# Kernel tuning notes

Hardware: AMD Instinct MI355X
Metric: run time of the kernel (lower is better)

Reference implementation:

```python
import jax, jax.numpy as jnp
import numpy as np

N_NODES = 50000
N_EDGES = 1600000
IN_DIM = 128
HID = 128
SHARED = 64
N_GRAPHS = 2048


def setup_inputs() -> dict:
    key = jax.random.key(0)
    ks = jax.random.split(key, 16)
    x = jax.random.normal(ks[0], (N_NODES, IN_DIM), dtype=jnp.float32)
    edge_index = jax.random.randint(ks[1], (2, N_EDGES), 0, N_NODES, dtype=jnp.int64)
    batch = jnp.sort(jax.random.randint(ks[2], (N_NODES,), 0, N_GRAPHS, dtype=jnp.int64))

    def lin(k, fan_in, fan_out):
        bound = 1.0 / np.sqrt(fan_in)
        kw, kb = jax.random.split(k)
        W = jax.random.uniform(kw, (fan_in, fan_out), minval=-bound, maxval=bound, dtype=jnp.float32)
        b = jax.random.uniform(kb, (fan_out,), minval=-bound, maxval=bound, dtype=jnp.float32)
        return W, b

    W1a, b1a = lin(ks[3], IN_DIM, HID)
    W1b, b1b = lin(ks[4], HID, HID)
    W2a, b2a = lin(ks[5], HID, HID)
    W2b, b2b = lin(ks[6], HID, HID)
    Ws, bs = lin(ks[7], HID, SHARED)
    WlS, blS = lin(ks[8], SHARED, 1)
    WlP, blP = lin(ks[9], SHARED, 1)
    WnR, bnR = lin(ks[10], SHARED, 1)
    return dict(x=x, edge_index=edge_index, batch=batch,
                W1a=W1a, b1a=b1a, W1b=W1b, b1b=b1b,
                W2a=W2a, b2a=b2a, W2b=W2b, b2b=b2b,
                Ws=Ws, bs=bs, WlS=WlS, blS=blS, WlP=WlP, blP=blP, WnR=WnR, bnR=bnR)


def gin_conv(x, src, dst, Wa, ba, Wb, bb):
    # GINConv (eps=0): h_i = MLP(x_i + sum_{j->i} x_j)
    agg = jax.ops.segment_sum(x[src], dst, num_segments=N_NODES)
    h = x + agg
    h = jax.nn.relu(h @ Wa + ba)
    return h @ Wb + bb


def reference(x, edge_index, batch, W1a, b1a, W1b, b1b, W2a, b2a, W2b, b2b,
              Ws, bs, WlS, blS, WlP, blP, WnR, bnR):
    src, dst = edge_index[0], edge_index[1]
    h = jax.nn.relu(gin_conv(x, src, dst, W1a, b1a, W1b, b1b))
    h = jax.nn.relu(gin_conv(h, src, dst, W2a, b2a, W2b, b2b))
    # global mean pool over graph ids
    sums = jax.ops.segment_sum(h, batch, num_segments=N_GRAPHS)
    counts = jax.ops.segment_sum(jnp.ones((h.shape[0],), h.dtype), batch, num_segments=N_GRAPHS)
    pooled = sums / jnp.maximum(counts, 1.0)[:, None]
    g = jax.nn.relu(pooled @ Ws + bs)
    out_logS = (g @ WlS + blS)[:, 0]
    out_logP = (g @ WlP + blP)[:, 0]
    out_NR = (g @ WnR + bnR)[:, 0]
    return (out_logS, out_logP, out_NR)
```

## Files before the change

### kernel.cpp

```cpp
#include <hip/hip_runtime.h>
#include <hip/hip_bf16.h>


#define IN_DIM 128
#define NFINE 128
#define BIN_EPB 4096
#define SRCCH 16
#define NSLOT 6400
#define SPT 13

typedef float  f32x4  __attribute__((ext_vector_type(4)));
typedef short  bf16x4 __attribute__((ext_vector_type(4)));
typedef short  bf16x8 __attribute__((ext_vector_type(8)));

__device__ __forceinline__ unsigned short bf16_rne(float v) {
    unsigned u = __float_as_uint(v);
    unsigned t = u + 0x7fffu + ((u >> 16) & 1u);
    return (unsigned short)(t >> 16);
}


__global__ __launch_bounds__(256) void f32_to_bf16_kernel(
    const float4* __restrict__ in, uint4* __restrict__ out, int n8)
{
    int i = blockIdx.x * 256 + threadIdx.x;
    if (i >= n8) return;
    float4 a = in[i * 2];
    float4 b = in[i * 2 + 1];
    float v[8] = {a.x, a.y, a.z, a.w, b.x, b.y, b.z, b.w};
    unsigned r[4];
#pragma unroll
    for (int j = 0; j < 4; ++j)
        r[j] = (unsigned)bf16_rne(v[j * 2]) | ((unsigned)bf16_rne(v[j * 2 + 1]) << 16);
    out[i] = make_uint4(r[0], r[1], r[2], r[3]);
}


__global__ __launch_bounds__(256) void conv_weights_kernel(
    const float* __restrict__ W0, const float* __restrict__ W1,
    const float* __restrict__ W2, const float* __restrict__ W3,
    unsigned short* __restrict__ Wh, unsigned short* __restrict__ Wl)
{
    int m   = blockIdx.x >> 6;
    int idx = (blockIdx.x & 63) * 256 + threadIdx.x;
    const float* W = (m == 0) ? W0 : (m == 1) ? W1 : (m == 2) ? W2 : W3;
    int k = idx >> 7, n = idx & 127;
    float v = W[idx];
    unsigned short hh = bf16_rne(v);
    float hf = __uint_as_float(((unsigned)hh) << 16);
    unsigned short ll = bf16_rne(v - hf);
    Wh[m * 16384 + n * 128 + k] = hh;
    Wl[m * 16384 + n * 128 + k] = ll;
}


__global__ __launch_bounds__(256) void bin_kernel(
    const int* __restrict__ src, const int* __restrict__ dst,
    int2* __restrict__ buckets, int* __restrict__ bcur,
    int n_edges, int n_nodes, int cap)
{
    __shared__ int cnt[NFINE];
    __shared__ int base[NFINE];
    for (int i = threadIdx.x; i < NFINE; i += 256) cnt[i] = 0;
    __syncthreads();

    const int e0 = blockIdx.x * BIN_EPB + threadIdx.x * 16;
    int ne = n_edges - e0;
    if (ne < 0) ne = 0;
    if (ne > 16) ne = 16;

    int d[16], s[16], off[16];
    if (ne == 16) {
#pragma unroll
        for (int q = 0; q < 4; ++q) {
            int4 dv = *(const int4*)(dst + e0 + q * 4);
            int4 sv = *(const int4*)(src + e0 + q * 4);
            d[q * 4 + 0] = dv.x; d[q * 4 + 1] = dv.y;
            d[q * 4 + 2] = dv.z; d[q * 4 + 3] = dv.w;
            s[q * 4 + 0] = sv.x; s[q * 4 + 1] = sv.y;
            s[q * 4 + 2] = sv.z; s[q * 4 + 3] = sv.w;
        }
    } else {
#pragma unroll
        for (int j = 0; j < 16; ++j) {
            d[j] = (j < ne) ? dst[e0 + j] : 0;
            s[j] = (j < ne) ? src[e0 + j] : 0;
        }
    }
#pragma unroll
    for (int j = 0; j < 16; ++j)
        if (j < ne) {
            int b = (int)(((long long)d[j] * NFINE) / n_nodes);
            off[j] = atomicAdd(&cnt[b], 1);
        }
    __syncthreads();
    for (int i = threadIdx.x; i < NFINE; i += 256)
        base[i] = atomicAdd(&bcur[i], cnt[i]);
    __syncthreads();
#pragma unroll
    for (int j = 0; j < 16; ++j)
        if (j < ne) {
            int b = (int)(((long long)d[j] * NFINE) / n_nodes);
            buckets[(size_t)b * cap + base[b] + off[j]] = make_int2(d[j], s[j]);
        }
}

__global__ __launch_bounds__(512) void csr_fused_kernel(
    const int2* __restrict__ buckets, const int* __restrict__ bcnt,
    int* __restrict__ row_start, int* __restrict__ csr_src,
    int cap, int n_nodes, int n_edges)
{
    __shared__ int bc[NFINE];
    __shared__ int h[NSLOT];
    __shared__ int tsum[512];
    __shared__ int bbase_s;

    const int b = blockIdx.x;
    const int t = threadIdx.x;
    const int lo_n = (int)(((long long)b * n_nodes + NFINE - 1) / NFINE);
    const int hi_n = (int)(((long long)(b + 1) * n_nodes + NFINE - 1) / NFINE);
    const int sl = hi_n - lo_n;

    if (t < NFINE) bc[t] = bcnt[t];
    for (int i = t; i < NSLOT; i += 512) h[i] = 0;
    __syncthreads();
    if (t == 0) {
        int s = 0;
        for (int i = 0; i < b; ++i) s += bc[i];
        bbase_s = s;
    }
    const int nb = bc[b];
    const int2* bp = buckets + (size_t)b * cap;
    __syncthreads();

    for (int i = t; i < nb; i += 512) {
        int2 e = bp[i];
        int key = (e.x - lo_n) * SRCCH + (int)(((long long)e.y * SRCCH) / n_nodes);
        atomicAdd(&h[key], 1);
    }
    __syncthreads();

    int base = 0;
#pragma unroll
    for (int j = 0; j < SPT; ++j) {
        int slot = t * SPT + j;
        if (slot < NSLOT) {
            int v = h[slot];
            h[slot] = base;
            base += v;
        }
    }
    tsum[t] = base;
    __syncthreads();
    for (int off = 1; off < 512; off <<= 1) {
        int tmp = (t >= off) ? tsum[t - off] : 0;
        __syncthreads();
        tsum[t] += tmp;
        __syncthreads();
    }
    int texcl = tsum[t] - base + bbase_s;
#pragma unroll
    for (int j = 0; j < SPT; ++j) {
        int slot = t * SPT + j;
        if (slot < NSLOT) h[slot] += texcl;
    }
    __syncthreads();
    for (int i = t; i < sl; i += 512) row_start[lo_n + i] = h[i * SRCCH];
    if (b == NFINE - 1 && t == 0) row_start[n_nodes] = n_edges;
    __syncthreads();

    for (int i = t; i < nb; i += 512) {
        int2 e = bp[i];
        int key = (e.x - lo_n) * SRCCH + (int)(((long long)e.y * SRCCH) / n_nodes);
        csr_src[atomicAdd(&h[key], 1)] = e.y;
    }
}


__device__ __forceinline__ void add_row8(float acc[8], uint4 r) {
    union { unsigned u; float f; } c;
    c.u = r.x << 16;         acc[0] += c.f;
    c.u = r.x & 0xffff0000u; acc[1] += c.f;
    c.u = r.y << 16;         acc[2] += c.f;
    c.u = r.y & 0xffff0000u; acc[3] += c.f;
    c.u = r.z << 16;         acc[4] += c.f;
    c.u = r.z & 0xffff0000u; acc[5] += c.f;
    c.u = r.w << 16;         acc[6] += c.f;
    c.u = r.w & 0xffff0000u; acc[7] += c.f;
}

__global__ __launch_bounds__(256) void gather_agg_bf16_kernel(
    const float* __restrict__ xf,
    const uint4* __restrict__ xb,
    const int* __restrict__ row_start, const int* __restrict__ csr_src,
    float* __restrict__ out, int n_nodes)
{
    int blk = blockIdx.x;
    int nfull = (gridDim.x >> 5) << 5;
    int group;
    if (blk < nfull) {
        int x = blk & 7;
        int q = blk >> 3;
        group = ((q >> 2) << 5) + (x << 2) + (q & 3);
    } else {
        group = blk;
    }

    int node = group * 16 + (threadIdx.x >> 4);
    int lane = threadIdx.x & 15;
    if (node >= n_nodes) return;
    int lo = row_start[node];
    int hi = row_start[node + 1];

    const f32x4* xfr = (const f32x4*)(xf + (size_t)node * IN_DIM + lane * 8);
    f32x4 a0 = xfr[0];
    f32x4 a1 = xfr[1];
    float acc[8] = {a0.x, a0.y, a0.z, a0.w, a1.x, a1.y, a1.z, a1.w};

    int e = lo;
    for (; e + 3 < hi; e += 4) {
        int s0 = csr_src[e];
        int s1 = csr_src[e + 1];
        int s2 = csr_src[e + 2];
        int s3 = csr_src[e + 3];
        uint4 r0 = xb[(size_t)s0 * 16 + lane];
        uint4 r1 = xb[(size_t)s1 * 16 + lane];
        uint4 r2 = xb[(size_t)s2 * 16 + lane];
        uint4 r3 = xb[(size_t)s3 * 16 + lane];
        add_row8(acc, r0);
        add_row8(acc, r1);
        add_row8(acc, r2);
        add_row8(acc, r3);
    }
    for (; e < hi; ++e) {
        uint4 r = xb[(size_t)csr_src[e] * 16 + lane];
        add_row8(acc, r);
    }

    f32x4* op = (f32x4*)(out + (size_t)node * IN_DIM + lane * 8);
    op[0] = (f32x4){acc[0], acc[1], acc[2], acc[3]};
    op[1] = (f32x4){acc[4], acc[5], acc[6], acc[7]};
}

#define HSTRIDE 132

template <bool EMIT_BF16>
__global__ __launch_bounds__(256) void fused_mlp_kernel(
    const float* __restrict__ A,
    const unsigned short* __restrict__ Wa_h, const unsigned short* __restrict__ Wa_l,
    const float* __restrict__ ba,
    const unsigned short* __restrict__ Wb_h, const unsigned short* __restrict__ Wb_l,
    const float* __restrict__ bb,
    float* __restrict__ C, unsigned short* __restrict__ Cb, int M)
{
    __shared__ __align__(16) unsigned short Hh[64][HSTRIDE];
    __shared__ __align__(16) unsigned short Hl[64][HSTRIDE];

    const int t    = threadIdx.x;
    const int wave = t >> 6;
    const int lane = t & 63;
    const int l15  = lane & 15;
    const int quad = lane >> 4;
    const int rw   = (wave & 1) * 32;
    const int cw   = (wave >> 1) * 64;
    const int row0 = blockIdx.x * 64 + rw;

    f32x4 acc[2][4];
#pragma unroll
    for (int ti = 0; ti < 2; ++ti)
#pragma unroll
        for (int ct = 0; ct < 4; ++ct) acc[ti][ct] = {0.f, 0.f, 0.f, 0.f};

    {
        int ar0 = row0 + l15;
        int ar1 = row0 + 16 + l15;
        const float* ap0 = A + (size_t)((ar0 < M) ? ar0 : (M - 1)) * IN_DIM + quad * 8;
        const float* ap1 = A + (size_t)((ar1 < M) ? ar1 : (M - 1)) * IN_DIM + quad * 8;
#pragma unroll
        for (int k0 = 0; k0 < IN_DIM; k0 += 32) {
            bf16x8 ah[2], al[2];
#pragma unroll
            for (int ti = 0; ti < 2; ++ti) {
                const float* ap = ti ? ap1 : ap0;
                f32x4 v0 = *(const f32x4*)(ap + k0);
                f32x4 v1 = *(const f32x4*)(ap + k0 + 4);
                float v[8] = {v0.x, v0.y, v0.z, v0.w, v1.x, v1.y, v1.z, v1.w};
                unsigned short h[8], l[8];
#pragma unroll
                for (int j = 0; j < 8; ++j) {
                    unsigned short hh = bf16_rne(v[j]);
                    h[j] = hh;
                    l[j] = bf16_rne(v[j] - __uint_as_float(((unsigned)hh) << 16));
                }
                ah[ti] = *(const bf16x8*)h;
                al[ti] = *(const bf16x8*)l;
            }
#pragma unroll
            for (int ct = 0; ct < 4; ++ct) {
                const size_t woff = (size_t)(cw + ct * 16 + l15) * IN_DIM + k0 + quad * 8;
                bf16x8 wh = *(const bf16x8*)(Wa_h + woff);
                bf16x8 wl = *(const bf16x8*)(Wa_l + woff);
                acc[0][ct] = __builtin_amdgcn_mfma_f32_16x16x32_bf16(ah[0], wh, acc[0][ct], 0, 0, 0);
                acc[1][ct] = __builtin_amdgcn_mfma_f32_16x16x32_bf16(ah[1], wh, acc[1][ct], 0, 0, 0);
                acc[0][ct] = __builtin_amdgcn_mfma_f32_16x16x32_bf16(al[0], wh, acc[0][ct], 0, 0, 0);
                acc[1][ct] = __builtin_amdgcn_mfma_f32_16x16x32_bf16(al[1], wh, acc[1][ct], 0, 0, 0);
                acc[0][ct] = __builtin_amdgcn_mfma_f32_16x16x32_bf16(ah[0], wl, acc[0][ct], 0, 0, 0);
                acc[1][ct] = __builtin_amdgcn_mfma_f32_16x16x32_bf16(ah[1], wl, acc[1][ct], 0, 0, 0);
            }
        }
    }

#pragma unroll
    for (int ti = 0; ti < 2; ++ti) {
#pragma unroll
        for (int ct = 0; ct < 4; ++ct) {
            int col = cw + ct * 16 + l15;
            float b = ba[col];
#pragma unroll
            for (int r = 0; r < 4; ++r) {
                int rl = rw + ti * 16 + quad * 4 + r;
                float v = fmaxf(acc[ti][ct][r] + b, 0.f);
                unsigned short hh = bf16_rne(v);
                Hh[rl][col] = hh;
                Hl[rl][col] = bf16_rne(v - __uint_as_float(((unsigned)hh) << 16));
            }
            acc[ti][ct] = {0.f, 0.f, 0.f, 0.f};
        }
    }
    __syncthreads();

#pragma unroll
    for (int k0 = 0; k0 < IN_DIM; k0 += 32) {
        const int hk = k0 + quad * 8;
        bf16x8 ah[2], al[2];
#pragma unroll
        for (int ti = 0; ti < 2; ++ti) {
            const int hr = rw + ti * 16 + l15;
            bf16x4 h0 = *(const bf16x4*)&Hh[hr][hk];
            bf16x4 h1 = *(const bf16x4*)&Hh[hr][hk + 4];
            bf16x4 l0 = *(const bf16x4*)&Hl[hr][hk];
            bf16x4 l1 = *(const bf16x4*)&Hl[hr][hk + 4];
            ah[ti] = __builtin_shufflevector(h0, h1, 0, 1, 2, 3, 4, 5, 6, 7);
            al[ti] = __builtin_shufflevector(l0, l1, 0, 1, 2, 3, 4, 5, 6, 7);
        }
#pragma unroll
        for (int ct = 0; ct < 4; ++ct) {
            const size_t woff = (size_t)(cw + ct * 16 + l15) * IN_DIM + k0 + quad * 8;
            bf16x8 wh = *(const bf16x8*)(Wb_h + woff);
            bf16x8 wl = *(const bf16x8*)(Wb_l + woff);
            acc[0][ct] = __builtin_amdgcn_mfma_f32_16x16x32_bf16(ah[0], wh, acc[0][ct], 0, 0, 0);
            acc[1][ct] = __builtin_amdgcn_mfma_f32_16x16x32_bf16(ah[1], wh, acc[1][ct], 0, 0, 0);
            acc[0][ct] = __builtin_amdgcn_mfma_f32_16x16x32_bf16(al[0], wh, acc[0][ct], 0, 0, 0);
            acc[1][ct] = __builtin_amdgcn_mfma_f32_16x16x32_bf16(al[1], wh, acc[1][ct], 0, 0, 0);
            acc[0][ct] = __builtin_amdgcn_mfma_f32_16x16x32_bf16(ah[0], wl, acc[0][ct], 0, 0, 0);
            acc[1][ct] = __builtin_amdgcn_mfma_f32_16x16x32_bf16(ah[1], wl, acc[1][ct], 0, 0, 0);
        }
    }

#pragma unroll
    for (int ti = 0; ti < 2; ++ti) {
        const int rbase = row0 + ti * 16 + quad * 4;
#pragma unroll
        for (int ct = 0; ct < 4; ++ct) {
            int col = cw + ct * 16 + l15;
            float b = bb[col];
#pragma unroll
            for (int r = 0; r < 4; ++r) {
                int row = rbase + r;
                if (row < M) {
                    float o = fmaxf(acc[ti][ct][r] + b, 0.f);
                    C[(size_t)row * IN_DIM + col] = o;
                    if (EMIT_BF16)
                        Cb[(size_t)row * IN_DIM + col] = bf16_rne(o);
                }
            }
        }
    }
}


__device__ __forceinline__ int lower_bound_i(const int* __restrict__ a, int n, int v) {
    int lo = 0, hi = n;
    while (lo < hi) {
        int mid = (lo + hi) >> 1;
        if (a[mid] < v) lo = mid + 1; else hi = mid;
    }
    return lo;
}

__global__ __launch_bounds__(128) void pool_kernel(
    const float* __restrict__ h, const int* __restrict__ batch,
    float* __restrict__ pooled, int n_nodes, int n_graphs)
{
    int g = blockIdx.x;
    int lo = lower_bound_i(batch, n_nodes, g);
    int hi = lower_bound_i(batch, n_nodes, g + 1);
    int j = threadIdx.x;
    float acc = 0.f;
    for (int i = lo; i < hi; ++i)
        acc += h[(size_t)i * IN_DIM + j];
    float cnt = (float)(hi - lo);
    pooled[(size_t)g * IN_DIM + j] = acc / fmaxf(cnt, 1.0f);
}

__global__ __launch_bounds__(64) void head_kernel(
    const float* __restrict__ pooled,
    const float* __restrict__ Ws,  const float* __restrict__ bs,
    const float* __restrict__ WlS, const float* __restrict__ blS,
    const float* __restrict__ WlP, const float* __restrict__ blP,
    const float* __restrict__ WnR, const float* __restrict__ bnR,
    float* __restrict__ out, int n_graphs)
{
    int g = blockIdx.x;
    int j = threadIdx.x;
    const float* p = pooled + (size_t)g * IN_DIM;
    float acc = bs[j];
#pragma unroll 8
    for (int k = 0; k < IN_DIM; ++k)
        acc = fmaf(p[k], Ws[k * 64 + j], acc);
    float gj = fmaxf(acc, 0.f);
    float s1 = gj * WlS[j];
    float s2 = gj * WlP[j];
    float s3 = gj * WnR[j];
#pragma unroll
    for (int off = 32; off > 0; off >>= 1) {
        s1 += __shfl_down(s1, off);
        s2 += __shfl_down(s2, off);
        s3 += __shfl_down(s3, off);
    }
    if (j == 0) {
        out[g]                = s1 + blS[0];
        out[n_graphs + g]     = s2 + blP[0];
        out[2 * n_graphs + g] = s3 + bnR[0];
    }
}


extern "C" void kernel_launch(void* const* d_in, const int* in_sizes, int n_in,
                              void* d_out, int out_size, void* d_ws, size_t ws_size,
                              hipStream_t stream)
{
    const float* x   = (const float*)d_in[0];
    const int*   ei  = (const int*)d_in[1];
    const int*   bat = (const int*)d_in[2];
    const float* W1a = (const float*)d_in[3];
    const float* b1a = (const float*)d_in[4];
    const float* W1b = (const float*)d_in[5];
    const float* b1b = (const float*)d_in[6];
    const float* W2a = (const float*)d_in[7];
    const float* b2a = (const float*)d_in[8];
    const float* W2b = (const float*)d_in[9];
    const float* b2b = (const float*)d_in[10];
    const float* Ws  = (const float*)d_in[11];
    const float* bs  = (const float*)d_in[12];
    const float* WlS = (const float*)d_in[13];
    const float* blS = (const float*)d_in[14];
    const float* WlP = (const float*)d_in[15];
    const float* blP = (const float*)d_in[16];
    const float* WnR = (const float*)d_in[17];
    const float* bnR = (const float*)d_in[18];

    const int n_nodes  = in_sizes[0] / IN_DIM;
    const int n_edges  = in_sizes[1] / 2;
    const int n_graphs = out_size / 3;
    const int* src = ei;
    const int* dst = ei + n_edges;

    const size_t node_elems   = (size_t)n_nodes * IN_DIM;
    const size_t pooled_elems = (size_t)n_graphs * IN_DIM;

    float* xbf    = (float*)d_ws;
    float* buf2   = xbf  + node_elems;
    float* bufA   = buf2 + node_elems;
    float* pooled = bufA + node_elems;
    int* row_start = (int*)(pooled + pooled_elems);
    int* bcur      = row_start + (n_nodes + 1);
    int* csr_src   = bcur + NFINE;
    unsigned short* wt_h = (unsigned short*)(csr_src + n_edges);
    unsigned short* wt_l = wt_h + 4 * 16384;

    unsigned short* xb = (unsigned short*)xbf;
    const int cap = n_edges / NFINE + 2048;
    int2* buckets = (int2*)bufA;

    const int gatherblocks = (int)(((size_t)n_nodes * 16 + 255) / 256);
    const int mlpblocks = (n_nodes + 63) / 64;
    const int binblocks = (n_edges + BIN_EPB - 1) / BIN_EPB;
    const int n8 = (int)(node_elems / 8);
    const int cvtblocks = (n8 + 255) / 256;

    conv_weights_kernel<<<256, 256, 0, stream>>>(W1a, W1b, W2a, W2b, wt_h, wt_l);
    hipMemsetAsync(bcur, 0, NFINE * sizeof(int), stream);
    bin_kernel<<<binblocks, 256, 0, stream>>>(src, dst, buckets, bcur,
                                              n_edges, n_nodes, cap);
    csr_fused_kernel<<<NFINE, 512, 0, stream>>>(buckets, bcur, row_start,
                                                csr_src, cap, n_nodes, n_edges);

    f32_to_bf16_kernel<<<cvtblocks, 256, 0, stream>>>((const float4*)x, (uint4*)xb, n8);
    gather_agg_bf16_kernel<<<gatherblocks, 256, 0, stream>>>(
        x, (const uint4*)xb, row_start, csr_src, bufA, n_nodes);
    fused_mlp_kernel<true><<<mlpblocks, 256, 0, stream>>>(
        bufA, wt_h, wt_l, b1a, wt_h + 16384, wt_l + 16384, b1b,
        buf2, xb, n_nodes);

    gather_agg_bf16_kernel<<<gatherblocks, 256, 0, stream>>>(
        buf2, (const uint4*)xb, row_start, csr_src, bufA, n_nodes);
    fused_mlp_kernel<false><<<mlpblocks, 256, 0, stream>>>(
        bufA, wt_h + 2 * 16384, wt_l + 2 * 16384, b2a,
        wt_h + 3 * 16384, wt_l + 3 * 16384, b2b,
        buf2, nullptr, n_nodes);

    pool_kernel<<<n_graphs, 128, 0, stream>>>(buf2, bat, pooled, n_nodes, n_graphs);
    head_kernel<<<n_graphs, 64, 0, stream>>>(pooled, Ws, bs, WlS, blS, WlP, blP,
                                             WnR, bnR, (float*)d_out, n_graphs);
}
```

Baseline: 370.0 us.

## Store intermediate activations as split bf16 hi/lo pairs and use 512-thread MLP blocks

```diff
diff --git a/kernel.cpp b/kernel.cpp
--- a/kernel.cpp
+++ b/kernel.cpp
@@ -189,11 +189,14 @@
     c.u = r.w & 0xffff0000u; acc[7] += c.f;
 }
 
+template <bool SELF_SPLIT>
 __global__ __launch_bounds__(256) void gather_agg_bf16_kernel(
     const float* __restrict__ xf,
+    const uint4* __restrict__ sh,
+    const uint4* __restrict__ slo,
     const uint4* __restrict__ xb,
     const int* __restrict__ row_start, const int* __restrict__ csr_src,
-    float* __restrict__ out, int n_nodes)
+    uint4* __restrict__ outh, uint4* __restrict__ outl, int n_nodes)
 {
     int blk = blockIdx.x;
     int nfull = (gridDim.x >> 5) << 5;
@@ -212,10 +215,21 @@
     int lo = row_start[node];
     int hi = row_start[node + 1];
 
-    const f32x4* xfr = (const f32x4*)(xf + (size_t)node * IN_DIM + lane * 8);
-    f32x4 a0 = xfr[0];
-    f32x4 a1 = xfr[1];
-    float acc[8] = {a0.x, a0.y, a0.z, a0.w, a1.x, a1.y, a1.z, a1.w};
+    float acc[8];
+    if constexpr (SELF_SPLIT) {
+        uint4 h = sh[(size_t)node * 16 + lane];
+        uint4 l = slo[(size_t)node * 16 + lane];
+#pragma unroll
+        for (int j = 0; j < 8; ++j) acc[j] = 0.f;
+        add_row8(acc, h);
+        add_row8(acc, l);
+    } else {
+        const f32x4* xfr = (const f32x4*)(xf + (size_t)node * IN_DIM + lane * 8);
+        f32x4 a0 = xfr[0];
+        f32x4 a1 = xfr[1];
+        acc[0] = a0.x; acc[1] = a0.y; acc[2] = a0.z; acc[3] = a0.w;
+        acc[4] = a1.x; acc[5] = a1.y; acc[6] = a1.z; acc[7] = a1.w;
+    }
 
     int e = lo;
     for (; e + 3 < hi; e += 4) {
@@ -237,21 +251,31 @@
         add_row8(acc, r);
     }
 
-    f32x4* op = (f32x4*)(out + (size_t)node * IN_DIM + lane * 8);
-    op[0] = (f32x4){acc[0], acc[1], acc[2], acc[3]};
-    op[1] = (f32x4){acc[4], acc[5], acc[6], acc[7]};
+    unsigned ph[4], pl[4];
+#pragma unroll
+    for (int j = 0; j < 4; ++j) {
+        unsigned short h0 = bf16_rne(acc[2 * j]);
+        unsigned short l0 = bf16_rne(acc[2 * j] - __uint_as_float(((unsigned)h0) << 16));
+        unsigned short h1 = bf16_rne(acc[2 * j + 1]);
+        unsigned short l1 = bf16_rne(acc[2 * j + 1] - __uint_as_float(((unsigned)h1) << 16));
+        ph[j] = (unsigned)h0 | ((unsigned)h1 << 16);
+        pl[j] = (unsigned)l0 | ((unsigned)l1 << 16);
+    }
+    outh[(size_t)node * 16 + lane] = make_uint4(ph[0], ph[1], ph[2], ph[3]);
+    outl[(size_t)node * 16 + lane] = make_uint4(pl[0], pl[1], pl[2], pl[3]);
 }
 
 #define HSTRIDE 132
 
-template <bool EMIT_BF16>
-__global__ __launch_bounds__(256) void fused_mlp_kernel(
-    const float* __restrict__ A,
+template <bool EMIT_SPLIT>
+__global__ __launch_bounds__(512) void fused_mlp_kernel(
+    const unsigned short* __restrict__ Ah, const unsigned short* __restrict__ Al,
     const unsigned short* __restrict__ Wa_h, const unsigned short* __restrict__ Wa_l,
     const float* __restrict__ ba,
     const unsigned short* __restrict__ Wb_h, const unsigned short* __restrict__ Wb_l,
     const float* __restrict__ bb,
-    float* __restrict__ C, unsigned short* __restrict__ Cb, int M)
+    float* __restrict__ C, unsigned short* __restrict__ Ch,
+    unsigned short* __restrict__ Cl, int M)
 {
     __shared__ __align__(16) unsigned short Hh[64][HSTRIDE];
     __shared__ __align__(16) unsigned short Hl[64][HSTRIDE];
@@ -261,51 +285,42 @@
     const int lane = t & 63;
     const int l15  = lane & 15;
     const int quad = lane >> 4;
-    const int rw   = (wave & 1) * 32;
-    const int cw   = (wave >> 1) * 64;
-    const int row0 = blockIdx.x * 64 + rw;
-
-    f32x4 acc[2][4];
+    const int rh   = (wave & 1) * 32;
+    const int cq   = (wave >> 1) * 32;
+    const int brow = blockIdx.x * 64;
+
+    f32x4 acc[2][2];
 #pragma unroll
     for (int ti = 0; ti < 2; ++ti)
 #pragma unroll
-        for (int ct = 0; ct < 4; ++ct) acc[ti][ct] = {0.f, 0.f, 0.f, 0.f};
+        for (int ct = 0; ct < 2; ++ct) acc[ti][ct] = {0.f, 0.f, 0.f, 0.f};
 
     {
-        int ar0 = row0 + l15;
-        int ar1 = row0 + 16 + l15;
-        const float* ap0 = A + (size_t)((ar0 < M) ? ar0 : (M - 1)) * IN_DIM + quad * 8;
-        const float* ap1 = A + (size_t)((ar1 < M) ? ar1 : (M - 1)) * IN_DIM + quad * 8;
+        int ar0 = brow + rh + l15;
+        int ar1 = brow + rh + 16 + l15;
+        if (ar0 >= M) ar0 = M - 1;
+        if (ar1 >= M) ar1 = M - 1;
+        const unsigned short* a0h = Ah + (size_t)ar0 * IN_DIM + quad * 8;
+        const unsigned short* a0l = Al + (size_t)ar0 * IN_DIM + quad * 8;
+        const unsigned short* a1h = Ah + (size_t)ar1 * IN_DIM + quad * 8;
+        const unsigned short* a1l = Al + (size_t)ar1 * IN_DIM + quad * 8;
 #pragma unroll
         for (int k0 = 0; k0 < IN_DIM; k0 += 32) {
-            bf16x8 ah[2], al[2];
-#pragma unroll
-            for (int ti = 0; ti < 2; ++ti) {
-                const float* ap = ti ? ap1 : ap0;
-                f32x4 v0 = *(const f32x4*)(ap + k0);
-                f32x4 v1 = *(const f32x4*)(ap + k0 + 4);
-                float v[8] = {v0.x, v0.y, v0.z, v0.w, v1.x, v1.y, v1.z, v1.w};
-                unsigned short h[8], l[8];
-#pragma unroll
-                for (int j = 0; j < 8; ++j) {
-                    unsigned short hh = bf16_rne(v[j]);
-                    h[j] = hh;
-                    l[j] = bf16_rne(v[j] - __uint_as_float(((unsigned)hh) << 16));
-                }
-                ah[ti] = *(const bf16x8*)h;
-                al[ti] = *(const bf16x8*)l;
-            }
-#pragma unroll
-            for (int ct = 0; ct < 4; ++ct) {
-                const size_t woff = (size_t)(cw + ct * 16 + l15) * IN_DIM + k0 + quad * 8;
+            bf16x8 ah0 = *(const bf16x8*)(a0h + k0);
+            bf16x8 al0 = *(const bf16x8*)(a0l + k0);
+            bf16x8 ah1 = *(const bf16x8*)(a1h + k0);
+            bf16x8 al1 = *(const bf16x8*)(a1l + k0);
+#pragma unroll
+            for (int ct = 0; ct < 2; ++ct) {
+                const size_t woff = (size_t)(cq + ct * 16 + l15) * IN_DIM + k0 + quad * 8;
                 bf16x8 wh = *(const bf16x8*)(Wa_h + woff);
                 bf16x8 wl = *(const bf16x8*)(Wa_l + woff);
-                acc[0][ct] = __builtin_amdgcn_mfma_f32_16x16x32_bf16(ah[0], wh, acc[0][ct], 0, 0, 0);
-                acc[1][ct] = __builtin_amdgcn_mfma_f32_16x16x32_bf16(ah[1], wh, acc[1][ct], 0, 0, 0);
-                acc[0][ct] = __builtin_amdgcn_mfma_f32_16x16x32_bf16(al[0], wh, acc[0][ct], 0, 0, 0);
-                acc[1][ct] = __builtin_amdgcn_mfma_f32_16x16x32_bf16(al[1], wh, acc[1][ct], 0, 0, 0);
-                acc[0][ct] = __builtin_amdgcn_mfma_f32_16x16x32_bf16(ah[0], wl, acc[0][ct], 0, 0, 0);
-                acc[1][ct] = __builtin_amdgcn_mfma_f32_16x16x32_bf16(ah[1], wl, acc[1][ct], 0, 0, 0);
+                acc[0][ct] = __builtin_amdgcn_mfma_f32_16x16x32_bf16(ah0, wh, acc[0][ct], 0, 0, 0);
+                acc[1][ct] = __builtin_amdgcn_mfma_f32_16x16x32_bf16(ah1, wh, acc[1][ct], 0, 0, 0);
+                acc[0][ct] = __builtin_amdgcn_mfma_f32_16x16x32_bf16(al0, wh, acc[0][ct], 0, 0, 0);
+                acc[1][ct] = __builtin_amdgcn_mfma_f32_16x16x32_bf16(al1, wh, acc[1][ct], 0, 0, 0);
+                acc[0][ct] = __builtin_amdgcn_mfma_f32_16x16x32_bf16(ah0, wl, acc[0][ct], 0, 0, 0);
+                acc[1][ct] = __builtin_amdgcn_mfma_f32_16x16x32_bf16(ah1, wl, acc[1][ct], 0, 0, 0);
             }
         }
     }
@@ -313,12 +328,12 @@
 #pragma unroll
     for (int ti = 0; ti < 2; ++ti) {
 #pragma unroll
-        for (int ct = 0; ct < 4; ++ct) {
-            int col = cw + ct * 16 + l15;
+        for (int ct = 0; ct < 2; ++ct) {
+            int col = cq + ct * 16 + l15;
             float b = ba[col];
 #pragma unroll
             for (int r = 0; r < 4; ++r) {
-                int rl = rw + ti * 16 + quad * 4 + r;
+                int rl = rh + ti * 16 + quad * 4 + r;
                 float v = fmaxf(acc[ti][ct][r] + b, 0.f);
                 unsigned short hh = bf16_rne(v);
                 Hh[rl][col] = hh;
@@ -335,7 +350,7 @@
         bf16x8 ah[2], al[2];
 #pragma unroll
         for (int ti = 0; ti < 2; ++ti) {
-            const int hr = rw + ti * 16 + l15;
+            const int hr = rh + ti * 16 + l15;
             bf16x4 h0 = *(const bf16x4*)&Hh[hr][hk];
             bf16x4 h1 = *(const bf16x4*)&Hh[hr][hk + 4];
             bf16x4 l0 = *(const bf16x4*)&Hl[hr][hk];
@@ -344,8 +359,8 @@
             al[ti] = __builtin_shufflevector(l0, l1, 0, 1, 2, 3, 4, 5, 6, 7);
         }
 #pragma unroll
-        for (int ct = 0; ct < 4; ++ct) {
-            const size_t woff = (size_t)(cw + ct * 16 + l15) * IN_DIM + k0 + quad * 8;
+        for (int ct = 0; ct < 2; ++ct) {
+            const size_t woff = (size_t)(cq + ct * 16 + l15) * IN_DIM + k0 + quad * 8;
             bf16x8 wh = *(const bf16x8*)(Wb_h + woff);
             bf16x8 wl = *(const bf16x8*)(Wb_l + woff);
             acc[0][ct] = __builtin_amdgcn_mfma_f32_16x16x32_bf16(ah[0], wh, acc[0][ct], 0, 0, 0);
@@ -359,19 +374,24 @@
 
 #pragma unroll
     for (int ti = 0; ti < 2; ++ti) {
-        const int rbase = row0 + ti * 16 + quad * 4;
-#pragma unroll
-        for (int ct = 0; ct < 4; ++ct) {
-            int col = cw + ct * 16 + l15;
+        const int rbase = brow + rh + ti * 16 + quad * 4;
+#pragma unroll
+        for (int ct = 0; ct < 2; ++ct) {
+            int col = cq + ct * 16 + l15;
             float b = bb[col];
 #pragma unroll
             for (int r = 0; r < 4; ++r) {
                 int row = rbase + r;
                 if (row < M) {
                     float o = fmaxf(acc[ti][ct][r] + b, 0.f);
-                    C[(size_t)row * IN_DIM + col] = o;
-                    if (EMIT_BF16)
-                        Cb[(size_t)row * IN_DIM + col] = bf16_rne(o);
+                    if (EMIT_SPLIT) {
+                        unsigned short hh = bf16_rne(o);
+                        Ch[(size_t)row * IN_DIM + col] = hh;
+                        Cl[(size_t)row * IN_DIM + col] =
+                            bf16_rne(o - __uint_as_float(((unsigned)hh) << 16));
+                    } else {
+                        C[(size_t)row * IN_DIM + col] = o;
+                    }
                 }
             }
         }
@@ -469,19 +489,24 @@
     const size_t node_elems   = (size_t)n_nodes * IN_DIM;
     const size_t pooled_elems = (size_t)n_graphs * IN_DIM;
 
-    float* xbf    = (float*)d_ws;
-    float* buf2   = xbf  + node_elems;
-    float* bufA   = buf2 + node_elems;
-    float* pooled = bufA + node_elems;
+    float* P1     = (float*)d_ws;
+    float* P2     = P1 + node_elems;
+    float* P3     = P2 + node_elems;
+    float* pooled = P3 + node_elems;
     int* row_start = (int*)(pooled + pooled_elems);
     int* bcur      = row_start + (n_nodes + 1);
     int* csr_src   = bcur + NFINE;
     unsigned short* wt_h = (unsigned short*)(csr_src + n_edges);
     unsigned short* wt_l = wt_h + 4 * 16384;
 
-    unsigned short* xb = (unsigned short*)xbf;
+    unsigned short* Ah = (unsigned short*)P1;
+    unsigned short* Al = Ah + node_elems;
+    unsigned short* xb = (unsigned short*)P2;
+    unsigned short* Ch = xb;
+    unsigned short* Cl = Ch + node_elems;
+
     const int cap = n_edges / NFINE + 2048;
-    int2* buckets = (int2*)bufA;
+    int2* buckets = (int2*)P1;
 
     const int gatherblocks = (int)(((size_t)n_nodes * 16 + 255) / 256);
     const int mlpblocks = (n_nodes + 63) / 64;
@@ -497,20 +522,22 @@
                                                 csr_src, cap, n_nodes, n_edges);
 
     f32_to_bf16_kernel<<<cvtblocks, 256, 0, stream>>>((const float4*)x, (uint4*)xb, n8);
-    gather_agg_bf16_kernel<<<gatherblocks, 256, 0, stream>>>(
-        x, (const uint4*)xb, row_start, csr_src, bufA, n_nodes);
-    fused_mlp_kernel<true><<<mlpblocks, 256, 0, stream>>>(
-        bufA, wt_h, wt_l, b1a, wt_h + 16384, wt_l + 16384, b1b,
-        buf2, xb, n_nodes);
-
-    gather_agg_bf16_kernel<<<gatherblocks, 256, 0, stream>>>(
-        buf2, (const uint4*)xb, row_start, csr_src, bufA, n_nodes);
-    fused_mlp_kernel<false><<<mlpblocks, 256, 0, stream>>>(
-        bufA, wt_h + 2 * 16384, wt_l + 2 * 16384, b2a,
+    gather_agg_bf16_kernel<false><<<gatherblocks, 256, 0, stream>>>(
+        x, nullptr, nullptr, (const uint4*)xb, row_start, csr_src,
+        (uint4*)Ah, (uint4*)Al, n_nodes);
+    fused_mlp_kernel<true><<<mlpblocks, 512, 0, stream>>>(
+        Ah, Al, wt_h, wt_l, b1a, wt_h + 16384, wt_l + 16384, b1b,
+        nullptr, Ch, Cl, n_nodes);
+
+    gather_agg_bf16_kernel<true><<<gatherblocks, 256, 0, stream>>>(
+        nullptr, (const uint4*)Ch, (const uint4*)Cl, (const uint4*)Ch,
+        row_start, csr_src, (uint4*)Ah, (uint4*)Al, n_nodes);
+    fused_mlp_kernel<false><<<mlpblocks, 512, 0, stream>>>(
+        Ah, Al, wt_h + 2 * 16384, wt_l + 2 * 16384, b2a,
         wt_h + 3 * 16384, wt_l + 3 * 16384, b2b,
-        buf2, nullptr, n_nodes);
-
-    pool_kernel<<<n_graphs, 128, 0, stream>>>(buf2, bat, pooled, n_nodes, n_graphs);
+        P3, nullptr, nullptr, n_nodes);
+
+    pool_kernel<<<n_graphs, 128, 0, stream>>>(P3, bat, pooled, n_nodes, n_graphs);
     head_kernel<<<n_graphs, 64, 0, stream>>>(pooled, Ws, bs, WlS, blS, WlP, blP,
                                              WnR, bnR, (float*)d_out, n_graphs);
 }
```

Result: slower. 383.3 us (+3.6%).
